# Optimization experiments

Hardware: AMD Instinct MI355X
Metric: run time of the kernel (lower is better)

Reference implementation:

```python
import jax, jax.numpy as jnp
import numpy as np

D_MODEL = 1024
NUM_HEADS = 16
HEAD_DIM = D_MODEL // NUM_HEADS
THETA = 10000.0
BATCH = 2
SEQ = 2048


def _apply_rope(x, positions):
    # x: (b, h, s, hd), positions: (b, s) int
    hd = x.shape[-1]
    inv_freq = 1.0 / (THETA ** (jnp.arange(0, hd, 2, dtype=jnp.float32) / hd))  # (hd/2,)
    ang = positions.astype(jnp.float32)[:, None, :, None] * inv_freq  # (b,1,s,hd/2)
    cos, sin = jnp.cos(ang), jnp.sin(ang)
    x1 = x[..., 0::2]
    x2 = x[..., 1::2]
    r1 = x1 * cos - x2 * sin
    r2 = x1 * sin + x2 * cos
    return jnp.stack([r1, r2], axis=-1).reshape(x.shape)


def setup_inputs() -> dict:
    key = jax.random.key(0)
    ks = jax.random.split(key, 5)
    scale = 1.0 / np.sqrt(D_MODEL)
    x = jax.random.normal(ks[0], (BATCH, SEQ, D_MODEL), dtype=jnp.float32)
    token_positions = jnp.broadcast_to(jnp.arange(SEQ, dtype=jnp.int32), (BATCH, SEQ))
    W_q = jax.random.normal(ks[1], (D_MODEL, D_MODEL), dtype=jnp.float32) * scale
    W_k = jax.random.normal(ks[2], (D_MODEL, D_MODEL), dtype=jnp.float32) * scale
    W_v = jax.random.normal(ks[3], (D_MODEL, D_MODEL), dtype=jnp.float32) * scale
    W_o = jax.random.normal(ks[4], (D_MODEL, D_MODEL), dtype=jnp.float32) * scale
    return {"x": x, "token_positions": token_positions, "W_q": W_q, "W_k": W_k, "W_v": W_v, "W_o": W_o}


def reference(x, token_positions, W_q, W_k, W_v, W_o):
    b, s, _ = x.shape
    h, hd = NUM_HEADS, HEAD_DIM
    # bias-free Linear: y = x @ W^T, W: (out, in)
    def proj(W):
        return jnp.einsum('bsd,ed->bse', x, W).reshape(b, s, h, hd).transpose(0, 2, 1, 3)
    Q = _apply_rope(proj(W_q), token_positions)
    K = _apply_rope(proj(W_k), token_positions)
    V = proj(W_v)
    scores = jnp.einsum('bhqd,bhkd->bhqk', Q, K) / jnp.sqrt(jnp.float32(hd))
    causal = jnp.triu(jnp.full((s, s), -jnp.inf, dtype=scores.dtype), k=1)
    attn = jax.nn.softmax(scores + causal, axis=-1)
    Z = jnp.einsum('bhqk,bhkd->bhqd', attn, V)
    Z = Z.transpose(0, 2, 1, 3).reshape(b, s, h * hd)
    return jnp.einsum('bse,de->bsd', Z, W_o)
```

## Files before the change

kernel.cpp:

```cpp
#include <hip/hip_runtime.h>
#include <hip/hip_bf16.h>


#define BATCH 2
#define SEQ   2048
#define NH    16
#define HD    64
#define DM    1024
#define MTOT  (BATCH*SEQ)

typedef __attribute__((ext_vector_type(8))) short bf16x8;
typedef __attribute__((ext_vector_type(4))) float f32x4;
typedef __attribute__((ext_vector_type(4))) unsigned int u32x4;
typedef unsigned short u16;
typedef unsigned int   u32;

__device__ __forceinline__ float b2f(u16 h){ return __uint_as_float(((u32)h) << 16); }
__device__ __forceinline__ u16 f2b(float f){
  u32 u = __float_as_uint(f);
  u32 r = (u + 0x7FFFu + ((u >> 16) & 1u)) >> 16;
  return (u16)r;
}
__device__ __forceinline__ u16 cvt1(float f){
  __hip_bfloat16 h = __float2bfloat16(f);
  return *reinterpret_cast<u16*>(&h);
}
__device__ __forceinline__ u32 pk2(float lo, float hi){
  return (u32)cvt1(lo) | ((u32)cvt1(hi) << 16);
}
__device__ __forceinline__ f32x4 mfma16(bf16x8 a, bf16x8 b, f32x4 c){
  return __builtin_amdgcn_mfma_f32_16x16x32_bf16(a, b, c, 0, 0, 0);
}
__device__ __forceinline__ void gload_lds16(const u16* g, u16* l){
  __builtin_amdgcn_global_load_lds((const __attribute__((address_space(1))) unsigned int*)g,
                                   (__attribute__((address_space(3))) unsigned int*)l, 16, 0, 0);
}

__global__ __launch_bounds__(256) void cvt_all(const float* __restrict__ x,
    const float* __restrict__ wq, const float* __restrict__ wk,
    const float* __restrict__ wv, const float* __restrict__ wo,
    u16* __restrict__ xb, u16* __restrict__ wb)
{
  const long NX = (long)MTOT * DM;
  const long NW = (long)DM * DM;
  const long tot4 = (NX + 4*NW) >> 2;
  for (long t = (long)blockIdx.x*blockDim.x + threadIdx.x; t < tot4;
       t += (long)gridDim.x*blockDim.x){
    long e = t << 2;
    const float* s; u16* d;
    if (e < NX){ s = x + e; d = xb + e; }
    else {
      long j = e - NX; int z = (int)(j >> 20);
      const float* ws = (z==0)?wq:(z==1)?wk:(z==2)?wv:wo;
      s = ws + (j & (NW-1)); d = wb + j;
    }
    float4 v = *(const float4*)s;
    u32 lo = (u32)f2b(v.x) | ((u32)f2b(v.y) << 16);
    u32 hi = (u32)f2b(v.z) | ((u32)f2b(v.w) << 16);
    uint2 o; o.x = lo; o.y = hi;
    *(uint2*)d = o;
  }
}

__global__ __launch_bounds__(256) void rope_table(float2* __restrict__ tab){
  int t = blockIdx.x*blockDim.x + threadIdx.x;
  if (t >= SEQ*32) return;
  int s = t >> 5, i = t & 31;
  float inv = 1.0f / powf(10000.0f, (float)i * (1.0f/32.0f));
  float a = (float)s * inv;
  tab[t] = make_float2(cosf(a), sinf(a));
}

__device__ __forceinline__ void gemm128_core(const u16* __restrict__ A, const u16* __restrict__ B,
    int mbase, int nbase, u16* Alds, u16* Blds, f32x4 acc[4][4])
{
  const int tid = threadIdx.x;
  const int w = tid >> 6, l = tid & 63, g = l >> 4, c = l & 15;
  const int wr = (w >> 1)*64, wc = (w & 1)*64;
  const int srow = l >> 3;
  const int scol = ((l & 7) ^ srow)*8;
  const u16* Ag = A + (long)(mbase + w*32 + srow)*DM + scol;
  const u16* Bg = B + (long)(nbase + w*32 + srow)*DM + scol;
  u16* Alb = Alds + w*2048;
  u16* Blb = Blds + w*2048;

  for (int k0 = 0; k0 < DM; k0 += 64){
    __syncthreads();
    #pragma unroll
    for (int i = 0; i < 4; i++){
      gload_lds16(Ag + k0 + (long)(8*i)*DM, Alb + i*512);
      gload_lds16(Bg + k0 + (long)(8*i)*DM, Blb + i*512);
    }
    __syncthreads();
    #pragma unroll
    for (int ks = 0; ks < 2; ks++){
      bf16x8 af[4], bfr[4];
      #pragma unroll
      for (int mi = 0; mi < 4; mi++){
        int row = wr + mi*16 + c;
        af[mi] = *(const bf16x8*)&Alds[row*64 + (((ks*4 + g) ^ (row & 7))*8)];
      }
      #pragma unroll
      for (int nj = 0; nj < 4; nj++){
        int row = wc + nj*16 + c;
        bfr[nj] = *(const bf16x8*)&Blds[row*64 + (((ks*4 + g) ^ (row & 7))*8)];
      }
      #pragma unroll
      for (int mi = 0; mi < 4; mi++)
        #pragma unroll
        for (int nj = 0; nj < 4; nj++)
          acc[mi][nj] = mfma16(af[mi], bfr[nj], acc[mi][nj]);
    }
  }
}

__global__ __launch_bounds__(256) void gemm_qkv(const u16* __restrict__ xb,
                                                const u16* __restrict__ wb,
                                                u16* __restrict__ qkvr)
{
  __shared__ u16 Alds[128*64];
  __shared__ u16 Blds[128*64];
  const int z = blockIdx.z;
  const u16* Bm = wb + (long)z * DM * DM;
  u16* C = qkvr + (long)z * MTOT * DM;
  const int nbase = blockIdx.x*128, mbase = blockIdx.y*128;
  const int w = threadIdx.x >> 6, l = threadIdx.x & 63, g = l >> 4, c = l & 15;
  const int wr = (w >> 1)*64, wc = (w & 1)*64;
  f32x4 acc[4][4] = {};
  gemm128_core(xb, Bm, mbase, nbase, Alds, Blds, acc);
  #pragma unroll
  for (int mi = 0; mi < 4; mi++)
    #pragma unroll
    for (int nj = 0; nj < 4; nj++)
      #pragma unroll
      for (int r = 0; r < 4; r++){
        int row = mbase + wr + mi*16 + 4*g + r;
        int col = nbase + wc + nj*16 + c;
        C[(long)row*DM + col] = f2b(acc[mi][nj][r]);
      }
}

__global__ __launch_bounds__(256) void gemm_out(const u16* __restrict__ Zb,
                                                const u16* __restrict__ wob,
                                                float* __restrict__ out)
{
  __shared__ u16 Alds[128*64];
  __shared__ u16 Blds[128*64];
  const int nbase = blockIdx.x*128, mbase = blockIdx.y*128;
  const int w = threadIdx.x >> 6, l = threadIdx.x & 63, g = l >> 4, c = l & 15;
  const int wr = (w >> 1)*64, wc = (w & 1)*64;
  f32x4 acc[4][4] = {};
  gemm128_core(Zb, wob, mbase, nbase, Alds, Blds, acc);
  #pragma unroll
  for (int mi = 0; mi < 4; mi++)
    #pragma unroll
    for (int nj = 0; nj < 4; nj++)
      #pragma unroll
      for (int r = 0; r < 4; r++){
        int row = mbase + wr + mi*16 + 4*g + r;
        int col = nbase + wc + nj*16 + c;
        out[(long)row*DM + col] = acc[mi][nj][r];
      }
}

__global__ __launch_bounds__(256) void rope_scatter(const u16* __restrict__ qkvr,
    u16* __restrict__ Qd, u16* __restrict__ Kd, u16* __restrict__ Vt,
    const float2* __restrict__ tab, const int* __restrict__ pos)
{
  int st = blockIdx.x, h = blockIdx.y, b = blockIdx.z;
  int s0 = st*64;
  const u16* Qraw = qkvr;
  const u16* Kraw = qkvr + (long)MTOT*DM;
  const u16* Vraw = qkvr + 2L*MTOT*DM;

  for (int t = threadIdx.x; t < 64*32; t += 256){
    int sl = t >> 5, i = t & 31;
    int s = s0 + sl;
    int p = pos[b*SEQ + s];
    if (p < 0) p = 0; if (p >= SEQ) p = SEQ - 1;
    float2 cs = tab[p*32 + i];
    long inoff  = (long)(b*SEQ + s)*DM + h*HD + 2*i;
    long outoff = ((long)(b*NH + h)*SEQ + s)*HD + 2*i;
    u32 qe = *(const u32*)(Qraw + inoff);
    float x1 = b2f((u16)(qe & 0xffff)), x2 = b2f((u16)(qe >> 16));
    float r1 = x1*cs.x - x2*cs.y;
    float r2 = x1*cs.y + x2*cs.x;
    *(u32*)(Qd + outoff) = (u32)f2b(r1) | ((u32)f2b(r2) << 16);
    u32 ke = *(const u32*)(Kraw + inoff);
    x1 = b2f((u16)(ke & 0xffff)); x2 = b2f((u16)(ke >> 16));
    r1 = x1*cs.x - x2*cs.y;
    r2 = x1*cs.y + x2*cs.x;
    *(u32*)(Kd + outoff) = (u32)f2b(r1) | ((u32)f2b(r2) << 16);
  }

  __shared__ u16 vt[64][65];
  for (int t = threadIdx.x; t < 64*8; t += 256){
    int sl = t >> 3, ch = (t & 7)*8;
    bf16x8 v = *(const bf16x8*)(Vraw + (long)(b*SEQ + s0 + sl)*DM + h*HD + ch);
    #pragma unroll
    for (int j = 0; j < 8; j++) vt[sl][ch + j] = (u16)v[j];
  }
  __syncthreads();
  for (int t = threadIdx.x; t < 64*8; t += 256){
    int d = t >> 3, ch = (t & 7)*8;
    bf16x8 v;
    #pragma unroll
    for (int j = 0; j < 8; j++) v[j] = (short)vt[ch + j][d];
    *(bf16x8*)(Vt + ((long)(b*NH + h)*HD + d)*SEQ + s0 + ch) = v;
  }
}

__device__ __forceinline__ int kperm(int a){
  return (a & 32) | ((a & 4) << 2) | ((a & 24) >> 1) | (a & 3);
}

__global__ __launch_bounds__(256) void attn(const u16* __restrict__ Q, const u16* __restrict__ K,
                                            const u16* __restrict__ Vt,
                                            u16* __restrict__ Opart, float2* __restrict__ ML)
{
  const int pair = (int)blockIdx.x >> 1;
  const int half = blockIdx.x & 1;
  const int h = blockIdx.y, b = blockIdx.z;
  const int tid = threadIdx.x, w = tid >> 6, l = tid & 63, g = l >> 4, c = l & 15;
  const u16* Kp = K  + (long)(b*NH + h)*SEQ*HD;
  const u16* Vp = Vt + (long)(b*NH + h)*HD*SEQ;

  __shared__ u16 K_lds[2][64][64];
  __shared__ u16 V_lds[2][64][64];

  const int srow0 = tid >> 3, sch = tid & 7;
  const int kpr0 = kperm(srow0), kpr1 = kperm(srow0 + 32);
  const int cswz = c & 7;
  const float SC = 0.125f * 1.44269504089f;

  int cur = 0;
  #pragma unroll 1
  for (int seg = 0; seg < 2; ++seg){
    const int qt = seg ? (31 - pair) : pair;
    const int qbase = qt*64;
    const int qrow = qbase + w*16;
    const u16* Qp = Q + ((long)(b*NH + h)*SEQ + qrow)*HD;
    bf16x8 qf0 = *(const bf16x8*)(Qp + c*HD + g*8);
    bf16x8 qf1 = *(const bf16x8*)(Qp + c*HD + 32 + g*8);

    const int ntH0  = (qt + 2) >> 1;
    const int tstart = half ? ntH0 : 0;
    const int tend   = half ? (qt + 1) : ntH0;

    f32x4 accz[4] = {};
    float m = -1e30f, lsum = 0.f;

    if (tstart < tend){
      __syncthreads();
      bf16x8 kr[2], vr[2];
      #pragma unroll
      for (int i = 0; i < 2; i++){
        int row = srow0 + i*32;
        kr[i] = *(const bf16x8*)(Kp + (long)(tstart*64 + row)*HD + sch*8);
        vr[i] = *(const bf16x8*)(Vp + (long)row*SEQ + tstart*64 + sch*8);
      }
      *(bf16x8*)&K_lds[cur][kpr0][(sch ^ (kpr0 & 7))*8] = kr[0];
      *(bf16x8*)&K_lds[cur][kpr1][(sch ^ (kpr1 & 7))*8] = kr[1];
      *(bf16x8*)&V_lds[cur][srow0][(sch ^ (srow0 & 7))*8] = vr[0];
      *(bf16x8*)&V_lds[cur][srow0+32][(sch ^ ((srow0+32) & 7))*8] = vr[1];

      for (int t = tstart; t < tend; ++t){
        const int kbase = t*64;
        __syncthreads();

        if (t < tend-1){
          const int nb = kbase + 64;
          #pragma unroll
          for (int i = 0; i < 2; i++){
            int row = srow0 + i*32;
            kr[i] = *(const bf16x8*)(Kp + (long)(nb + row)*HD + sch*8);
            vr[i] = *(const bf16x8*)(Vp + (long)row*SEQ + nb + sch*8);
          }
        }

        f32x4 s[4];
        __builtin_amdgcn_s_setprio(1);
        #pragma unroll
        for (int sub = 0; sub < 4; sub++){
          int row = sub*16 + c;
          bf16x8 ka0 = *(const bf16x8*)&K_lds[cur][row][((0+g) ^ cswz)*8];
          bf16x8 ka1 = *(const bf16x8*)&K_lds[cur][row][((4+g) ^ cswz)*8];
          f32x4 z4 = {};
          z4 = mfma16(ka0, qf0, z4);
          z4 = mfma16(ka1, qf1, z4);
          s[sub] = z4;
        }
        __builtin_amdgcn_s_setprio(0);

        const bool edge = (kbase + 63 > qrow);
        const int q = qrow + c;
        #pragma unroll
        for (int sub = 0; sub < 4; sub++)
          #pragma unroll
          for (int r = 0; r < 4; r++){
            float v = s[sub][r]*SC;
            if (edge){
              int key = kbase + ((sub >> 1) << 5) + 8*g + ((sub & 1) << 2) + r;
              if (key > q) v = -1e30f;
            }
            s[sub][r] = v;
          }

        float tmax = s[0][0];
        #pragma unroll
        for (int sub = 0; sub < 4; sub++)
          #pragma unroll
          for (int r = 0; r < 4; r++) tmax = fmaxf(tmax, s[sub][r]);
        tmax = fmaxf(tmax, __shfl_xor(tmax, 16));
        tmax = fmaxf(tmax, __shfl_xor(tmax, 32));

        if (!__all(tmax <= m + 8.f)){
          float nm = fmaxf(m, tmax);
          float f = exp2f(m - nm);
          m = nm;
          lsum *= f;
          float f_bc[4];
          #pragma unroll
          for (int r = 0; r < 4; r++) f_bc[r] = __shfl(f, 4*g + r);
          #pragma unroll
          for (int dt = 0; dt < 4; dt++)
            #pragma unroll
            for (int r = 0; r < 4; r++) accz[dt][r] *= f_bc[r];
        }

        float psum = 0.f;
        #pragma unroll
        for (int sub = 0; sub < 4; sub++)
          #pragma unroll
          for (int r = 0; r < 4; r++){
            float e = exp2f(s[sub][r] - m);
            s[sub][r] = e;
            psum += e;
          }
        psum += __shfl_xor(psum, 16);
        psum += __shfl_xor(psum, 32);
        lsum += psum;

        u32x4 p0, p1;
        p0[0] = pk2(s[0][0], s[0][1]); p0[1] = pk2(s[0][2], s[0][3]);
        p0[2] = pk2(s[1][0], s[1][1]); p0[3] = pk2(s[1][2], s[1][3]);
        p1[0] = pk2(s[2][0], s[2][1]); p1[1] = pk2(s[2][2], s[2][3]);
        p1[2] = pk2(s[3][0], s[3][1]); p1[3] = pk2(s[3][2], s[3][3]);
        bf16x8 pf0 = __builtin_bit_cast(bf16x8, p0);
        bf16x8 pf1 = __builtin_bit_cast(bf16x8, p1);

        __builtin_amdgcn_s_setprio(1);
        #pragma unroll
        for (int dt = 0; dt < 4; dt++){
          int vrow = dt*16 + c;
          bf16x8 vf0 = *(const bf16x8*)&V_lds[cur][vrow][((0+g) ^ cswz)*8];
          bf16x8 vf1 = *(const bf16x8*)&V_lds[cur][vrow][((4+g) ^ cswz)*8];
          accz[dt] = mfma16(pf0, vf0, accz[dt]);
          accz[dt] = mfma16(pf1, vf1, accz[dt]);
        }
        __builtin_amdgcn_s_setprio(0);

        if (t < tend-1){
          int nx = cur ^ 1;
          *(bf16x8*)&K_lds[nx][kpr0][(sch ^ (kpr0 & 7))*8] = kr[0];
          *(bf16x8*)&K_lds[nx][kpr1][(sch ^ (kpr1 & 7))*8] = kr[1];
          *(bf16x8*)&V_lds[nx][srow0][(sch ^ (srow0 & 7))*8] = vr[0];
          *(bf16x8*)&V_lds[nx][srow0+32][(sch ^ ((srow0+32) & 7))*8] = vr[1];
          cur = nx;
        }
      }
    }

    const int pbase = (((b*NH + h)*32 + qt)*2 + half);
    if (g == 0)
      ML[pbase*64 + w*16 + c] = make_float2(m, lsum);
    u16* Op = Opart + (long)pbase*(64*64);
    #pragma unroll
    for (int dt = 0; dt < 4; dt++)
      #pragma unroll
      for (int r = 0; r < 4; r++)
        Op[(w*16 + 4*g + r)*64 + dt*16 + c] = cvt1(accz[dt][r]);
  }
}

__global__ __launch_bounds__(256) void attn_combine(const u16* __restrict__ Opart,
                                                    const float2* __restrict__ ML,
                                                    u16* __restrict__ Z)
{
  const int qt = blockIdx.x, h = blockIdx.y, b = blockIdx.z;
  const int p0 = ((b*NH + h)*32 + qt)*2, p1 = p0 + 1;
  const int row = threadIdx.x >> 2;
  const int d0  = (threadIdx.x & 3)*16;
  float2 ml0 = ML[p0*64 + row];
  float2 ml1 = ML[p1*64 + row];
  float M = fmaxf(ml0.x, ml1.x);
  float w0 = exp2f(ml0.x - M), w1 = exp2f(ml1.x - M);
  float inv = 1.f / (ml0.y*w0 + ml1.y*w1);
  float a0 = w0*inv, a1 = w1*inv;
  const u16* o0 = Opart + ((long)p0*64 + row)*64 + d0;
  const u16* o1 = Opart + ((long)p1*64 + row)*64 + d0;
  const int s = qt*64 + row;
  u16* zp = Z + (long)(b*SEQ + s)*DM + h*HD + d0;
  #pragma unroll
  for (int j = 0; j < 2; j++){
    bf16x8 va = *(const bf16x8*)(o0 + j*8);
    bf16x8 vb = *(const bf16x8*)(o1 + j*8);
    bf16x8 ov;
    #pragma unroll
    for (int e = 0; e < 8; e++){
      float z = b2f((u16)va[e])*a0 + b2f((u16)vb[e])*a1;
      ov[e] = (short)cvt1(z);
    }
    *(bf16x8*)(zp + j*8) = ov;
  }
}

extern "C" void kernel_launch(void* const* d_in, const int* in_sizes, int n_in,
                              void* d_out, int out_size, void* d_ws, size_t ws_size,
                              hipStream_t stream)
{
  const float* x  = (const float*)d_in[0];
  const int*   pos= (const int*)d_in[1];
  const float* wq = (const float*)d_in[2];
  const float* wk = (const float*)d_in[3];
  const float* wv = (const float*)d_in[4];
  const float* wo = (const float*)d_in[5];
  float* out = (float*)d_out;

  const long NX = (long)MTOT*DM;
  const long NW = (long)DM*DM;
  char* p = (char*)d_ws;
  u16* xb   = (u16*)p;  p += NX*2;
  u16* wb   = (u16*)p;  p += 4*NW*2;
  u16* qkvr = (u16*)p;  p += 3*NX*2;
  u16* Qd   = (u16*)p;  p += NX*2;
  u16* Kd   = (u16*)p;  p += NX*2;
  u16* Vt   = (u16*)p;  p += NX*2;
  u16* Zb   = (u16*)p;  p += NX*2;
  float2* tab = (float2*)p; p += (long)SEQ*32*sizeof(float2);
  u16* Opart = (u16*)p;  p += 2L*NX*2;
  float2* ML = (float2*)p; p += 2048L*64*sizeof(float2);
  (void)ws_size; (void)n_in; (void)in_sizes; (void)out_size;

  hipLaunchKernelGGL(cvt_all,     dim3(2048),      dim3(256), 0, stream, x, wq, wk, wv, wo, xb, wb);
  hipLaunchKernelGGL(rope_table,  dim3(256),       dim3(256), 0, stream, tab);
  hipLaunchKernelGGL(gemm_qkv,    dim3(8,32,3),    dim3(256), 0, stream, xb, wb, qkvr);
  hipLaunchKernelGGL(rope_scatter,dim3(32,16,2),   dim3(256), 0, stream, qkvr, Qd, Kd, Vt, tab, pos);
  hipLaunchKernelGGL(attn,        dim3(32,16,2),   dim3(256), 0, stream, Qd, Kd, Vt, Opart, ML);
  hipLaunchKernelGGL(attn_combine,dim3(32,16,2),   dim3(256), 0, stream, Opart, ML, Zb);
  hipLaunchKernelGGL(gemm_out,    dim3(8,32),      dim3(256), 0, stream, Zb, wb + 3*NW, out);
}
```

Measured before the change: 137.9 us.

## Fold softmax scale into Q and compute row sums via MFMA with ones

The softmax scale (1/sqrt(hd)·log2e) is now applied to Q during the RoPE scatter pass, which removes a per-score multiply from the attention inner loop. The masking loop now runs only on edge tiles. The per-row exp sum is no longer a scalar reduction with cross-lane shuffles; it is accumulated by two extra MFMAs of P against a ones vector, and the result is read from the accumulator layout when writing ML. This trades VALU and shuffle work for extra matrix-core work. It sums the bf16-rounded P, which keeps the denominator consistent with the numerator, and it rounds the scaled Q to bf16, which slightly changes precision.

```diff
diff --git a/kernel.cpp b/kernel.cpp
--- a/kernel.cpp
+++ b/kernel.cpp
@@ -172,6 +172,7 @@
   const u16* Qraw = qkvr;
   const u16* Kraw = qkvr + (long)MTOT*DM;
   const u16* Vraw = qkvr + 2L*MTOT*DM;
+  const float SC = 0.125f * 1.44269504089f;
 
   for (int t = threadIdx.x; t < 64*32; t += 256){
     int sl = t >> 5, i = t & 31;
@@ -183,8 +184,8 @@
     long outoff = ((long)(b*NH + h)*SEQ + s)*HD + 2*i;
     u32 qe = *(const u32*)(Qraw + inoff);
     float x1 = b2f((u16)(qe & 0xffff)), x2 = b2f((u16)(qe >> 16));
-    float r1 = x1*cs.x - x2*cs.y;
-    float r2 = x1*cs.y + x2*cs.x;
+    float r1 = (x1*cs.x - x2*cs.y)*SC;
+    float r2 = (x1*cs.y + x2*cs.x)*SC;
     *(u32*)(Qd + outoff) = (u32)f2b(r1) | ((u32)f2b(r2) << 16);
     u32 ke = *(const u32*)(Kraw + inoff);
     x1 = b2f((u16)(ke & 0xffff)); x2 = b2f((u16)(ke >> 16));
@@ -231,7 +232,10 @@
   const int srow0 = tid >> 3, sch = tid & 7;
   const int kpr0 = kperm(srow0), kpr1 = kperm(srow0 + 32);
   const int cswz = c & 7;
-  const float SC = 0.125f * 1.44269504089f;
+
+  bf16x8 ones;
+  #pragma unroll
+  for (int j = 0; j < 8; j++) ones[j] = (short)0x3F80;
 
   int cur = 0;
   #pragma unroll 1
@@ -248,7 +252,8 @@
     const int tend   = half ? (qt + 1) : ntH0;
 
     f32x4 accz[4] = {};
-    float m = -1e30f, lsum = 0.f;
+    f32x4 lacc = {};
+    float m = -1e30f;
 
     if (tstart < tend){
       __syncthreads();
@@ -294,23 +299,21 @@
 
         const bool edge = (kbase + 63 > qrow);
         const int q = qrow + c;
-        #pragma unroll
-        for (int sub = 0; sub < 4; sub++)
-          #pragma unroll
-          for (int r = 0; r < 4; r++){
-            float v = s[sub][r]*SC;
-            if (edge){
+        if (edge){
+          #pragma unroll
+          for (int sub = 0; sub < 4; sub++)
+            #pragma unroll
+            for (int r = 0; r < 4; r++){
               int key = kbase + ((sub >> 1) << 5) + 8*g + ((sub & 1) << 2) + r;
-              if (key > q) v = -1e30f;
+              if (key > q) s[sub][r] = -1e30f;
             }
-            s[sub][r] = v;
-          }
-
-        float tmax = s[0][0];
-        #pragma unroll
-        for (int sub = 0; sub < 4; sub++)
-          #pragma unroll
-          for (int r = 0; r < 4; r++) tmax = fmaxf(tmax, s[sub][r]);
+        }
+
+        float a0 = fmaxf(fmaxf(s[0][0], s[0][1]), fmaxf(s[0][2], s[0][3]));
+        float a1 = fmaxf(fmaxf(s[1][0], s[1][1]), fmaxf(s[1][2], s[1][3]));
+        float a2 = fmaxf(fmaxf(s[2][0], s[2][1]), fmaxf(s[2][2], s[2][3]));
+        float a3 = fmaxf(fmaxf(s[3][0], s[3][1]), fmaxf(s[3][2], s[3][3]));
+        float tmax = fmaxf(fmaxf(a0, a1), fmaxf(a2, a3));
         tmax = fmaxf(tmax, __shfl_xor(tmax, 16));
         tmax = fmaxf(tmax, __shfl_xor(tmax, 32));
 
@@ -318,28 +321,22 @@
           float nm = fmaxf(m, tmax);
           float f = exp2f(m - nm);
           m = nm;
-          lsum *= f;
           float f_bc[4];
           #pragma unroll
           for (int r = 0; r < 4; r++) f_bc[r] = __shfl(f, 4*g + r);
+          #pragma unroll
+          for (int r = 0; r < 4; r++) lacc[r] *= f_bc[r];
           #pragma unroll
           for (int dt = 0; dt < 4; dt++)
             #pragma unroll
             for (int r = 0; r < 4; r++) accz[dt][r] *= f_bc[r];
         }
 
-        float psum = 0.f;
         #pragma unroll
         for (int sub = 0; sub < 4; sub++)
           #pragma unroll
-          for (int r = 0; r < 4; r++){
-            float e = exp2f(s[sub][r] - m);
-            s[sub][r] = e;
-            psum += e;
-          }
-        psum += __shfl_xor(psum, 16);
-        psum += __shfl_xor(psum, 32);
-        lsum += psum;
+          for (int r = 0; r < 4; r++)
+            s[sub][r] = exp2f(s[sub][r] - m);
 
         u32x4 p0, p1;
         p0[0] = pk2(s[0][0], s[0][1]); p0[1] = pk2(s[0][2], s[0][3]);
@@ -350,6 +347,8 @@
         bf16x8 pf1 = __builtin_bit_cast(bf16x8, p1);
 
         __builtin_amdgcn_s_setprio(1);
+        lacc = mfma16(pf0, ones, lacc);
+        lacc = mfma16(pf1, ones, lacc);
         #pragma unroll
         for (int dt = 0; dt < 4; dt++){
           int vrow = dt*16 + c;
@@ -372,8 +371,14 @@
     }
 
     const int pbase = (((b*NH + h)*32 + qt)*2 + half);
-    if (g == 0)
-      ML[pbase*64 + w*16 + c] = make_float2(m, lsum);
+    float m_bc[4];
+    #pragma unroll
+    for (int r = 0; r < 4; r++) m_bc[r] = __shfl(m, 4*g + r);
+    if (c == 0){
+      #pragma unroll
+      for (int r = 0; r < 4; r++)
+        ML[pbase*64 + w*16 + 4*g + r] = make_float2(m_bc[r], lacc[r]);
+    }
     u16* Op = Opart + (long)pbase*(64*64);
     #pragma unroll
     for (int dt = 0; dt < 4; dt++)
```

Measured after the change: 132.6 us. 3.9% less time.
